# Optimization experiments

Measured on AMD Instinct MI355X. Metric: run time of the kernel, lower is better.

## Reference

```python
import jax, jax.numpy as jnp
import numpy as np
from jax import lax

B_, N_, DIM, HID, DST, NT, IR, DTR, HH, WW = 16, 4096, 192, 384, 16, 17, 128, 24, 64, 64


def _selective_scan(u, delta, A, Bs, Cs, D, delta_bias):
    # u, delta: (B, Din, L); A: (Din, N); Bs, Cs: (B, N, L); D, delta_bias: (Din,)
    delta = jax.nn.softplus(delta + delta_bias[None, :, None])
    dT = jnp.moveaxis(delta, 2, 0)   # (L, B, Din)
    uT = jnp.moveaxis(u, 2, 0)       # (L, B, Din)
    BT = jnp.moveaxis(Bs, 2, 0)      # (L, B, N)
    CT = jnp.moveaxis(Cs, 2, 0)      # (L, B, N)
    Bsz, Din, L = u.shape
    Nst = A.shape[1]
    h0 = jnp.zeros((Bsz, Din, Nst), u.dtype)

    def step(h, inp):
        d_l, u_l, b_l, c_l = inp
        da = jnp.exp(d_l[:, :, None] * A[None])              # (B, Din, N)
        h = da * h + (d_l * u_l)[:, :, None] * b_l[:, None, :]
        y = jnp.einsum('bdn,bn->bd', h, c_l)
        return h, y

    _, ys = lax.scan(step, h0, (dT, uT, BT, CT))
    y = jnp.moveaxis(ys, 0, 2)                               # (B, Din, L)
    return y + u * D[None, :, None]


def _assm_forward(x, token_weight, gumbel_noise, embB, route_w1, route_b1, route_w2,
                  route_b2, inproj_w, inproj_b, cpe_w, cpe_b, x_proj_w, dt_w, dt_b,
                  A_logs, Ds, norm_g, norm_b, outproj_w, outproj_b, H, W, gather_type):
    B, n, C = x.shape
    hidden = inproj_w.shape[0]
    dst = token_weight.shape[1]
    dtr = dt_w.shape[1]

    # routing + gumbel-softmax (hard, straight-through)
    full_emb = embB @ token_weight                           # (NT, d_state)
    hmid = jax.nn.gelu(x @ route_w1.T + route_b1)
    logits = jax.nn.log_softmax(hmid @ route_w2.T + route_b2, axis=-1)
    y_soft = jax.nn.softmax(logits + gumbel_noise, axis=-1)
    idx = jnp.argmax(y_soft, axis=-1)                        # (B, n)
    y_hard = jax.nn.one_hot(idx, logits.shape[-1], dtype=y_soft.dtype)
    cls_policy = y_hard + y_soft - lax.stop_gradient(y_soft)
    prompt = cls_policy @ full_emb                           # (B, n, d_state)

    det = lax.stop_gradient(idx)
    # (gather_type 3/5 keypoint-group remap omitted: gather_type == 1 here)
    sort_idx = jnp.argsort(det, axis=-1)                     # (B, n)
    inv_idx = jnp.argsort(sort_idx, axis=-1)                 # index_reverse

    # in_proj (1x1 conv == pointwise linear) then depthwise CPE gate
    xi = x @ inproj_w.T + inproj_b                           # (B, n, hidden)
    xg = xi.reshape(B, H, W, hidden).transpose(0, 3, 1, 2)   # NCHW
    cpe = lax.conv_general_dilated(xg, cpe_w, (1, 1), 'SAME',
                                   feature_group_count=hidden,
                                   dimension_numbers=('NCHW', 'OIHW', 'NCHW'))
    cpe = cpe + cpe_b[None, :, None, None]
    xg = xg * jax.nn.sigmoid(cpe)
    xflat = xg.reshape(B, hidden, n).transpose(0, 2, 1)      # (B, n, hidden)

    sem_x = jnp.take_along_axis(xflat, sort_idx[:, :, None], axis=1)

    # Selective_Scan core
    xs = sem_x.transpose(0, 2, 1)                            # (B, Din, L)
    x_dbl = jnp.einsum('bdl,cd->bcl', xs, x_proj_w)          # (B, dtr+2N, L)
    dts, Bs, Cs = jnp.split(x_dbl, [dtr, dtr + dst], axis=1)
    dts = jnp.einsum('brl,dr->bdl', dts, dt_w)
    if gather_type != 0:
        Cs = Cs + prompt.transpose(0, 2, 1)
    A = -jnp.exp(A_logs)
    y = _selective_scan(xs, dts, A, Bs, Cs, Ds, dt_b)        # (B, Din, L)
    y = y.transpose(0, 2, 1)                                 # (B, L, hidden)

    mu = jnp.mean(y, axis=-1, keepdims=True)
    var = jnp.mean(jnp.square(y - mu), axis=-1, keepdims=True)
    yn = (y - mu) / jnp.sqrt(var + 1e-5) * norm_g + norm_b
    out = yn @ outproj_w.T + outproj_b                       # (B, n, dim)
    out = jnp.take_along_axis(out, inv_idx[:, :, None], axis=1)
    return out


def setup_inputs() -> dict:
    key = jax.random.key(0)
    ks = jax.random.split(key, 16)

    def rn(k, sh, s=0.02):
        return jax.random.normal(k, sh, dtype=jnp.float32) * s

    u = jax.random.uniform(ks[0], (B_, N_, NT), jnp.float32, 1e-6, 1.0 - 1e-6)
    gumbel = -jnp.log(-jnp.log(u))

    # faithful dt bias init (inverse-softplus of log-uniform dt)
    rng = np.random.default_rng(0)
    dt = np.exp(rng.uniform(size=HID) * (np.log(0.1) - np.log(0.001)) + np.log(0.001))
    dt = np.clip(dt, 1e-4, None)
    inv_dt = dt + np.log(-np.expm1(-dt))

    A_logs = jnp.log(jnp.tile(jnp.arange(1, DST + 1, dtype=jnp.float32), (HID, 1)))

    return {
        'x': jax.random.normal(ks[1], (B_, N_, DIM), jnp.float32),
        'token_weight': rn(ks[2], (IR, DST), 0.1),
        'gumbel_noise': gumbel,
        'embB': jax.random.uniform(ks[3], (NT, IR), jnp.float32, -1.0 / NT, 1.0 / NT),
        'route_w1': rn(ks[4], (DIM // 3, DIM)),
        'route_b1': jnp.zeros((DIM // 3,), jnp.float32),
        'route_w2': rn(ks[5], (NT, DIM // 3)),
        'route_b2': jnp.zeros((NT,), jnp.float32),
        'inproj_w': rn(ks[6], (HID, DIM)),
        'inproj_b': jnp.zeros((HID,), jnp.float32),
        'cpe_w': rn(ks[7], (HID, 1, 3, 3), 0.1),
        'cpe_b': jnp.zeros((HID,), jnp.float32),
        'x_proj_w': rn(ks[8], (DTR + 2 * DST, HID)),
        'dt_w': jax.random.uniform(ks[9], (HID, DTR), jnp.float32, -DTR ** -0.5, DTR ** -0.5),
        'dt_b': jnp.asarray(inv_dt, jnp.float32),
        'A_logs': A_logs,
        'Ds': jnp.ones((HID,), jnp.float32),
        'norm_g': jnp.ones((HID,), jnp.float32),
        'norm_b': jnp.zeros((HID,), jnp.float32),
        'outproj_w': rn(ks[10], (DIM, HID)),
        'outproj_b': jnp.zeros((DIM,), jnp.float32),
        'H': HH,
        'W': WW,
        'gather_type': 1,
    }


def reference(x, token_weight, gumbel_noise, embB, route_w1, route_b1, route_w2,
              route_b2, inproj_w, inproj_b, cpe_w, cpe_b, x_proj_w, dt_w, dt_b,
              A_logs, Ds, norm_g, norm_b, outproj_w, outproj_b, H, W, gather_type):
    return _assm_forward(x, token_weight, gumbel_noise, embB, route_w1, route_b1,
                         route_w2, route_b2, inproj_w, inproj_b, cpe_w, cpe_b,
                         x_proj_w, dt_w, dt_b, A_logs, Ds, norm_g, norm_b,
                         outproj_w, outproj_b, H, W, gather_type)
```

## Files before the change

### kernel.cpp

```cpp
#include <hip/hip_runtime.h>
#include <math.h>

#define NB 16
#define NL 4096
#define ND 192
#define NH 384
#define NS 16
#define NTK 17
#define NIR 128
#define NR 24
#define NHH 64
#define NWW 64
#define NCHUNKS 64
#define CHUNKLEN 64
#define NTOK (NB*NL)

typedef __attribute__((ext_vector_type(8))) short short8;
typedef __attribute__((ext_vector_type(4))) float floatx4;

__device__ __forceinline__ float gelu_tanh(float x){
  return 0.5f*x*(1.0f + tanhf(0.7978845608028654f*(x + 0.044715f*x*x*x)));
}
__device__ __forceinline__ float softplus_f(float x){
  return (x > 20.0f) ? x : log1pf(expf(x));
}
__device__ __forceinline__ short f2bf(float f){
  unsigned u = __float_as_uint(f);
  unsigned r = (u + 0x7fffu + ((u >> 16) & 1u)) >> 16;
  return (short)r;
}

union Pack8 { uint4 v; short s[8]; };

__global__ void k_emb(const float* __restrict__ embB, const float* __restrict__ tw,
                      float* __restrict__ fe){
  for (int o = threadIdx.x; o < NTK*NS; o += 256){
    int t = o / NS, s = o % NS;
    float acc = 0.f;
    for (int i = 0; i < NIR; ++i) acc += embB[t*NIR+i]*tw[i*NS+s];
    fe[o] = acc;
  }
}

__global__ void k_cvtw(const float* __restrict__ inw, const float* __restrict__ ow,
                       const float* __restrict__ xpw, const float* __restrict__ dtw,
                       short* __restrict__ inwb, short* __restrict__ owb,
                       short* __restrict__ xpwb, short* __restrict__ dtwb){
  int i = blockIdx.x*256 + threadIdx.x;
  int stride = gridDim.x*256;
  for (int p = i; p < NH*ND; p += stride) inwb[p] = f2bf(inw[p]);
  for (int p = i; p < ND*NH; p += stride) owb[p] = f2bf(ow[p]);
  for (int p = i; p < 56*NH; p += stride) xpwb[p] = f2bf(xpw[p]);
  for (int p = i; p < NH*32; p += stride){
    int r = p >> 5, c = p & 31;
    dtwb[p] = (c < NR) ? f2bf(dtw[r*NR + c]) : (short)0;
  }
}

template<int EPI>
__global__ __launch_bounds__(256) void k_gemm(const float* __restrict__ A, int lda,
    const float* __restrict__ W, int ldw, const float* __restrict__ bias,
    float* __restrict__ C, int ldc, int N, int K){
  __shared__ float As[16][68];
  __shared__ float Ws[16][68];
  int tid = threadIdx.x;
  int m0 = blockIdx.x*64, n0 = blockIdx.y*64;
  int tx = tid & 15, ty = tid >> 4;
  int srow = tid >> 2, skseg = (tid & 3)*4;
  float acc[4][4] = {};
  for (int k0 = 0; k0 < K; k0 += 16){
    {
      const float* ap = A + (size_t)(m0+srow)*lda + k0 + skseg;
      float4 v = *(const float4*)ap;
      As[skseg+0][srow]=v.x; As[skseg+1][srow]=v.y;
      As[skseg+2][srow]=v.z; As[skseg+3][srow]=v.w;
    }
    {
      float4 v = {0.f,0.f,0.f,0.f};
      if (n0 + srow < N) v = *(const float4*)(W + (size_t)(n0+srow)*ldw + k0 + skseg);
      Ws[skseg+0][srow]=v.x; Ws[skseg+1][srow]=v.y;
      Ws[skseg+2][srow]=v.z; Ws[skseg+3][srow]=v.w;
    }
    __syncthreads();
    #pragma unroll
    for (int kk = 0; kk < 16; ++kk){
      float4 av = *(const float4*)&As[kk][ty*4];
      float4 wv = *(const float4*)&Ws[kk][tx*4];
      acc[0][0] += av.x*wv.x; acc[0][1] += av.x*wv.y;
      acc[0][2] += av.x*wv.z; acc[0][3] += av.x*wv.w;
      acc[1][0] += av.y*wv.x; acc[1][1] += av.y*wv.y;
      acc[1][2] += av.y*wv.z; acc[1][3] += av.y*wv.w;
      acc[2][0] += av.z*wv.x; acc[2][1] += av.z*wv.y;
      acc[2][2] += av.z*wv.z; acc[2][3] += av.z*wv.w;
      acc[3][0] += av.w*wv.x; acc[3][1] += av.w*wv.y;
      acc[3][2] += av.w*wv.z; acc[3][3] += av.w*wv.w;
    }
    __syncthreads();
  }
  #pragma unroll
  for (int i = 0; i < 4; ++i){
    int m = m0 + ty*4 + i;
    #pragma unroll
    for (int j = 0; j < 4; ++j){
      int n = n0 + tx*4 + j;
      if (n < N){
        float v = acc[i][j] + (bias ? bias[n] : 0.f);
        if (EPI==1) v = gelu_tanh(v);
        C[(size_t)m*ldc + n] = v;
      }
    }
  }
}

template<int EPI, int AF32, int LNA>
__global__ __launch_bounds__(256) void k_mfma(const void* __restrict__ Aptr, int lda,
    const short* __restrict__ Wbf, int ldw, const float* __restrict__ bias,
    float* __restrict__ C, int ldc, int N, int K, const int* __restrict__ remap,
    const float* __restrict__ lnm, const float* __restrict__ lnr,
    const float* __restrict__ lng, const float* __restrict__ lnb){
  __shared__ short As[128*40];
  __shared__ short Bs[64*40];
  int tid = threadIdx.x;
  int m0 = blockIdx.x*128, n0 = blockIdx.y*64;
  int w = tid >> 6, lane = tid & 63;
  int lq = lane >> 4, lr = lane & 15;
  floatx4 acc[2][4];
  #pragma unroll
  for (int i = 0; i < 2; ++i)
    #pragma unroll
    for (int j = 0; j < 4; ++j) acc[i][j] = (floatx4){0.f,0.f,0.f,0.f};
  int ar = tid >> 1, aq = (tid & 1)*2;
  int br = tid >> 2, bq = tid & 3;
  float mr = 0.f, rr = 0.f;
  if (LNA){ mr = lnm[m0+ar]; rr = lnr[m0+ar]; }
  for (int k0 = 0; k0 < K; k0 += 32){
    Pack8 sa0, sa1;
    if (AF32){
      const float* ap = (const float*)Aptr + (size_t)(m0+ar)*lda + k0 + aq*8;
      float f[16];
      float4 f0 = *(const float4*)(ap);
      float4 f1 = *(const float4*)(ap+4);
      float4 f2 = *(const float4*)(ap+8);
      float4 f3 = *(const float4*)(ap+12);
      f[0]=f0.x; f[1]=f0.y; f[2]=f0.z; f[3]=f0.w;
      f[4]=f1.x; f[5]=f1.y; f[6]=f1.z; f[7]=f1.w;
      f[8]=f2.x; f[9]=f2.y; f[10]=f2.z; f[11]=f2.w;
      f[12]=f3.x; f[13]=f3.y; f[14]=f3.z; f[15]=f3.w;
      if (LNA){
        const float* gp = lng + k0 + aq*8;
        const float* bp = lnb + k0 + aq*8;
        #pragma unroll
        for (int j = 0; j < 16; ++j) f[j] = (f[j]-mr)*rr*gp[j] + bp[j];
      }
      #pragma unroll
      for (int j = 0; j < 8; ++j){ sa0.s[j] = f2bf(f[j]); sa1.s[j] = f2bf(f[8+j]); }
    } else {
      const short* ap = (const short*)Aptr + (size_t)(m0+ar)*lda + k0 + aq*8;
      sa0.v = *(const uint4*)ap;
      sa1.v = *(const uint4*)(ap + 8);
    }
    uint4 bv = {0u,0u,0u,0u};
    if (n0 + br < N) bv = *(const uint4*)(Wbf + (size_t)(n0+br)*ldw + k0 + bq*8);
    __syncthreads();
    *(uint4*)&As[ar*40 + aq*8]     = sa0.v;
    *(uint4*)&As[ar*40 + aq*8 + 8] = sa1.v;
    *(uint4*)&Bs[br*40 + bq*8]     = bv;
    __syncthreads();
    short8 a0 = *(const short8*)&As[(w*32      + lr)*40 + lq*8];
    short8 a1 = *(const short8*)&As[(w*32 + 16 + lr)*40 + lq*8];
    short8 b0 = *(const short8*)&Bs[(     lr)*40 + lq*8];
    short8 b1 = *(const short8*)&Bs[(16 + lr)*40 + lq*8];
    short8 b2 = *(const short8*)&Bs[(32 + lr)*40 + lq*8];
    short8 b3 = *(const short8*)&Bs[(48 + lr)*40 + lq*8];
    acc[0][0] = __builtin_amdgcn_mfma_f32_16x16x32_bf16(a0, b0, acc[0][0], 0,0,0);
    acc[0][1] = __builtin_amdgcn_mfma_f32_16x16x32_bf16(a0, b1, acc[0][1], 0,0,0);
    acc[0][2] = __builtin_amdgcn_mfma_f32_16x16x32_bf16(a0, b2, acc[0][2], 0,0,0);
    acc[0][3] = __builtin_amdgcn_mfma_f32_16x16x32_bf16(a0, b3, acc[0][3], 0,0,0);
    acc[1][0] = __builtin_amdgcn_mfma_f32_16x16x32_bf16(a1, b0, acc[1][0], 0,0,0);
    acc[1][1] = __builtin_amdgcn_mfma_f32_16x16x32_bf16(a1, b1, acc[1][1], 0,0,0);
    acc[1][2] = __builtin_amdgcn_mfma_f32_16x16x32_bf16(a1, b2, acc[1][2], 0,0,0);
    acc[1][3] = __builtin_amdgcn_mfma_f32_16x16x32_bf16(a1, b3, acc[1][3], 0,0,0);
  }
  #pragma unroll
  for (int mt = 0; mt < 2; ++mt){
    #pragma unroll
    for (int r = 0; r < 4; ++r){
      int m = m0 + w*32 + mt*16 + lq*4 + r;
      int orow = (EPI==3) ? remap[m] : m;
      #pragma unroll
      for (int nt = 0; nt < 4; ++nt){
        int n = n0 + nt*16 + lr;
        if (n < N){
          float v = acc[mt][nt][r] + (bias ? bias[n] : 0.f);
          if (EPI==2) v = softplus_f(v);
          C[(size_t)orow*ldc + n] = v;
        }
      }
    }
  }
}

__global__ __launch_bounds__(256) void k_argmax(const float* __restrict__ hmid,
    const float* __restrict__ w2, const float* __restrict__ b2,
    const float* __restrict__ gumbel, int* __restrict__ idx){
  int g = blockIdx.x*256 + threadIdx.x;
  float hm[64];
  const float4* hp = (const float4*)(hmid + (size_t)g*64);
  #pragma unroll
  for (int i = 0; i < 16; ++i){
    float4 v = hp[i];
    hm[i*4+0]=v.x; hm[i*4+1]=v.y; hm[i*4+2]=v.z; hm[i*4+3]=v.w;
  }
  float best = -INFINITY; int bi = 0;
  for (int c = 0; c < NTK; ++c){
    float s = b2[c] + gumbel[(size_t)g*NTK + c];
    #pragma unroll
    for (int j = 0; j < 64; ++j) s += hm[j]*w2[c*64+j];
    if (s > best){ best = s; bi = c; }
  }
  idx[g] = bi;
}

__global__ __launch_bounds__(256) void k_sort(const int* __restrict__ idx,
    int* __restrict__ rmap, int* __restrict__ inv){
  int b = blockIdx.x, t = threadIdx.x;
  __shared__ int hist[NTK][256];
  __shared__ int tot[NTK];
  __shared__ int keybase[NTK];
  int keys[16];
  const int* ip = idx + b*NL + t*16;
  #pragma unroll
  for (int i = 0; i < 16; ++i) keys[i] = ip[i];
  #pragma unroll
  for (int k = 0; k < NTK; ++k){
    int c = 0;
    #pragma unroll
    for (int i = 0; i < 16; ++i) c += (keys[i]==k) ? 1 : 0;
    hist[k][t] = c;
  }
  __syncthreads();
  if (t < NTK){
    int run = 0;
    for (int j = 0; j < 256; ++j){ int v = hist[t][j]; hist[t][j] = run; run += v; }
    tot[t] = run;
  }
  __syncthreads();
  if (t == 0){
    int base = 0;
    for (int k = 0; k < NTK; ++k){ keybase[k] = base; base += tot[k]; }
  }
  __syncthreads();
  #pragma unroll
  for (int i = 0; i < 16; ++i){
    int k = keys[i];
    int cb = 0;
    #pragma unroll
    for (int j = 0; j < 16; ++j) cb += (j < i && keys[j]==k) ? 1 : 0;
    int pos = keybase[k] + hist[k][t] + cb;
    rmap[b*NL + pos] = b*NL + t*16 + i;
    inv[b*NL + t*16 + i] = pos;
  }
}

__global__ __launch_bounds__(384) void k_cpe(const float* __restrict__ xi,
    const float* __restrict__ cw, const float* __restrict__ cb,
    const int* __restrict__ inv, float* __restrict__ us){
  int bl = blockIdx.x;
  int cg = bl & 3;
  int xt = (bl>>2) & 7;
  int yt = (bl>>5) & 7;
  int b  = bl >> 8;
  __shared__ float tile[10*10*96];
  int tx = threadIdx.x;
  int ty = threadIdx.y;
  int c0 = cg*96;
  int ch = c0 + tx;
  for (int yy = 0; yy < 10; ++yy){
    int gy = yt*8 + yy - 1;
    for (int xx = ty; xx < 10; xx += 4){
      int gx = xt*8 + xx - 1;
      float v = 0.f;
      if (gy >= 0 && gy < NHH && gx >= 0 && gx < NWW)
        v = xi[((size_t)(b*NL + gy*NWW + gx))*NH + ch];
      tile[(yy*10 + xx)*96 + tx] = v;
    }
  }
  float wreg[9];
  #pragma unroll
  for (int j = 0; j < 9; ++j) wreg[j] = cw[ch*9 + j];
  float bias = cb[ch];
  __syncthreads();
  for (int yy = ty; yy < 8; yy += 4){
    #pragma unroll
    for (int xx = 0; xx < 8; ++xx){
      float acc = bias;
      #pragma unroll
      for (int dy = 0; dy < 3; ++dy)
        #pragma unroll
        for (int dx = 0; dx < 3; ++dx)
          acc += tile[((yy+dy)*10 + (xx+dx))*96 + tx] * wreg[dy*3+dx];
      float center = tile[((yy+1)*10 + (xx+1))*96 + tx];
      float gate = 1.f/(1.f + expf(-acc));
      int l = (yt*8+yy)*NWW + xt*8+xx;
      int pos = inv[b*NL + l];
      us[((size_t)(b*NL + pos))*NH + ch] = center*gate;
    }
  }
}

__global__ __launch_bounds__(256) void k_bc(const float* __restrict__ dbl,
    const int* __restrict__ idx, const float* __restrict__ fe,
    const int* __restrict__ gt, float* __restrict__ Bsb, float* __restrict__ Csb,
    short* __restrict__ dtsb){
  int g = blockIdx.x*256 + threadIdx.x;
  const float* dr = dbl + (size_t)g*56;
  int id = idx[g];
  int gather = gt[0];
  #pragma unroll
  for (int n = 0; n < NR; ++n) dtsb[(size_t)g*32 + n] = f2bf(dr[n]);
  #pragma unroll
  for (int n = NR; n < 32; ++n) dtsb[(size_t)g*32 + n] = 0;
  #pragma unroll
  for (int n = 0; n < NS; ++n){
    Bsb[(size_t)g*NS + n] = dr[24+n];
    float c = dr[40+n];
    if (gather != 0) c += fe[id*NS + n];
    Csb[(size_t)g*NS + n] = c;
  }
}

__device__ __forceinline__ void decay16(bool pw, float dlt, const float* An, float* a){
  if (pw){
    float r  = __expf(dlt*An[0]);
    float r2 = r*r;
    float r3 = r2*r;
    float r4 = r2*r2;
    float r8 = r4*r4;
    float r12 = r8*r4;
    a[0]=r;     a[1]=r2;     a[2]=r3;     a[3]=r4;
    a[4]=r4*r;  a[5]=r4*r2;  a[6]=r4*r3;  a[7]=r8;
    a[8]=r8*r;  a[9]=r8*r2;  a[10]=r8*r3; a[11]=r12;
    a[12]=r12*r; a[13]=r12*r2; a[14]=r12*r3; a[15]=r8*r8;
  } else {
    #pragma unroll
    for (int n = 0; n < NS; ++n) a[n] = __expf(dlt*An[n]);
  }
}
__device__ __forceinline__ bool pwcheck(const float* An){
  bool pw = true;
  #pragma unroll
  for (int n = 1; n < NS; ++n)
    pw = pw && (fabsf(An[n] - (n+1)*An[0]) <= 1e-4f*fabsf(An[n]));
  return pw;
}

__global__ __launch_bounds__(384) void k_scan1(const float* __restrict__ delta,
    const float* __restrict__ us, const float* __restrict__ Bsb,
    const float* __restrict__ A_logs, float* __restrict__ sds, float* __restrict__ Boff){
  int bc = blockIdx.x;
  int c = bc & (NCHUNKS-1);
  int b = bc >> 6;
  int d = threadIdx.x;
  __shared__ float4 Bsh[CHUNKLEN*4];
  int base = b*NL + c*CHUNKLEN;
  {
    const float4* Bg = (const float4*)(Bsb + (size_t)base*NS);
    for (int p = d; p < CHUNKLEN*4; p += 384) Bsh[p] = Bg[p];
  }
  float An[NS];
  #pragma unroll
  for (int n = 0; n < NS; ++n) An[n] = -expf(A_logs[d*NS + n]);
  bool pw = pwcheck(An);
  float h[NS];
  #pragma unroll
  for (int n = 0; n < NS; ++n) h[n]=0.f;
  float sd = 0.f;
  __syncthreads();
  size_t gi = (size_t)base*NH + d;
  float dlt = delta[gi];
  float uv  = us[gi];
  #pragma unroll 2
  for (int s = 0; s < CHUNKLEN; ++s){
    float dltc = dlt, uvc = uv;
    if (s < CHUNKLEN-1){
      dlt = delta[gi + NH];
      uv  = us[gi + NH];
    }
    float du = dltc*uvc;
    sd += dltc;
    float a[NS];
    decay16(pw, dltc, An, a);
    float bb[NS];
    #pragma unroll
    for (int q = 0; q < 4; ++q) *(float4*)&bb[4*q] = Bsh[s*4 + q];
    #pragma unroll
    for (int n = 0; n < NS; ++n) h[n] = a[n]*h[n] + du*bb[n];
    gi += NH;
  }
  sds[(size_t)bc*NH + d] = sd;
  size_t o = ((size_t)bc*NH + d)*NS;
  #pragma unroll
  for (int n = 0; n < NS; ++n) Boff[o+n] = h[n];
}

__global__ __launch_bounds__(256) void k_scan2(const float* __restrict__ A_logs,
    const float* __restrict__ sds, float* __restrict__ Boff){
  int i = blockIdx.x*256 + threadIdx.x;
  int dn = i % (NH*NS);
  int b = i / (NH*NS);
  float An = -expf(A_logs[dn]);
  float h = 0.f;
  for (int c = 0; c < NCHUNKS; ++c){
    int bc = b*NCHUNKS + c;
    float sd = sds[(size_t)bc*NH + (dn >> 4)];
    float a = __expf(sd*An);
    size_t o = (size_t)bc*(NH*NS) + dn;
    float bo = Boff[o];
    Boff[o] = h;
    h = a*h + bo;
  }
}

__global__ __launch_bounds__(384) void k_scan3(const float* __restrict__ delta,
    const float* __restrict__ Bsb, const float* __restrict__ Csb,
    const float* __restrict__ A_logs, const float* __restrict__ Ds,
    const float* __restrict__ hinit, float* __restrict__ us){
  int bc = blockIdx.x;
  int c = bc & (NCHUNKS-1);
  int b = bc >> 6;
  int d = threadIdx.x;
  __shared__ float4 Bsh[CHUNKLEN*4];
  __shared__ float4 Csh[CHUNKLEN*4];
  int base = b*NL + c*CHUNKLEN;
  {
    const float4* Bg = (const float4*)(Bsb + (size_t)base*NS);
    const float4* Cg = (const float4*)(Csb + (size_t)base*NS);
    for (int p = d; p < CHUNKLEN*4; p += 384){
      Bsh[p] = Bg[p];
      Csh[p] = Cg[p];
    }
  }
  float An[NS];
  #pragma unroll
  for (int n = 0; n < NS; ++n) An[n] = -expf(A_logs[d*NS + n]);
  bool pw = pwcheck(An);
  float h[NS];
  size_t ho = ((size_t)bc*NH + d)*NS;
  #pragma unroll
  for (int n = 0; n < NS; ++n) h[n] = hinit[ho + n];
  float Dd = Ds[d];
  __syncthreads();
  size_t gi = (size_t)base*NH + d;
  float dlt = delta[gi];
  float uv  = us[gi];
  #pragma unroll 2
  for (int s = 0; s < CHUNKLEN; ++s){
    float dltc = dlt, uvc = uv;
    if (s < CHUNKLEN-1){
      dlt = delta[gi + NH];
      uv  = us[gi + NH];
    }
    float du = dltc*uvc;
    float a[NS];
    decay16(pw, dltc, An, a);
    float bb[NS], cc[NS];
    #pragma unroll
    for (int q = 0; q < 4; ++q){
      *(float4*)&bb[4*q] = Bsh[s*4 + q];
      *(float4*)&cc[4*q] = Csh[s*4 + q];
    }
    #pragma unroll
    for (int n = 0; n < NS; ++n) h[n] = a[n]*h[n] + du*bb[n];
    float ya = 0.f, yb = 0.f, yc = 0.f, yd = 0.f;
    #pragma unroll
    for (int q = 0; q < 4; ++q){
      ya += h[q]*cc[q];
      yb += h[4+q]*cc[4+q];
      yc += h[8+q]*cc[8+q];
      yd += h[12+q]*cc[12+q];
    }
    float y = (ya+yb)+(yc+yd);
    us[gi] = y + uvc*Dd;
    gi += NH;
  }
}

__global__ __launch_bounds__(256) void k_lnstat(const float* __restrict__ y,
    float* __restrict__ mean, float* __restrict__ rstd){
  int g = blockIdx.x*4 + (threadIdx.x >> 6);
  int lane = threadIdx.x & 63;
  size_t ro = (size_t)g*NH;
  float v[6];
  #pragma unroll
  for (int i = 0; i < 6; ++i) v[i] = y[ro + i*64 + lane];
  float s = 0.f;
  #pragma unroll
  for (int i = 0; i < 6; ++i) s += v[i];
  #pragma unroll
  for (int off = 32; off > 0; off >>= 1) s += __shfl_xor(s, off);
  float mu = s * (1.f/NH);
  float vs = 0.f;
  #pragma unroll
  for (int i = 0; i < 6; ++i){ float d = v[i]-mu; vs += d*d; }
  #pragma unroll
  for (int off = 32; off > 0; off >>= 1) vs += __shfl_xor(vs, off);
  float rs = rsqrtf(vs*(1.f/NH) + 1e-5f);
  if (lane == 0){ mean[g] = mu; rstd[g] = rs; }
}

extern "C" void kernel_launch(void* const* d_in, const int* in_sizes, int n_in,
                              void* d_out, int out_size, void* d_ws, size_t ws_size,
                              hipStream_t stream){
  const float* x      = (const float*)d_in[0];
  const float* tw     = (const float*)d_in[1];
  const float* gumbel = (const float*)d_in[2];
  const float* embB   = (const float*)d_in[3];
  const float* rw1    = (const float*)d_in[4];
  const float* rb1    = (const float*)d_in[5];
  const float* rw2    = (const float*)d_in[6];
  const float* rb2    = (const float*)d_in[7];
  const float* inw    = (const float*)d_in[8];
  const float* inb    = (const float*)d_in[9];
  const float* cw     = (const float*)d_in[10];
  const float* cb     = (const float*)d_in[11];
  const float* xpw    = (const float*)d_in[12];
  const float* dtw    = (const float*)d_in[13];
  const float* dtb    = (const float*)d_in[14];
  const float* A_logs = (const float*)d_in[15];
  const float* Ds     = (const float*)d_in[16];
  const float* ng     = (const float*)d_in[17];
  const float* nbv    = (const float*)d_in[18];
  const float* ow     = (const float*)d_in[19];
  const float* ob     = (const float*)d_in[20];
  const int*   gt     = (const int*)d_in[23];
  float* out = (float*)d_out;

  float* ws = (float*)d_ws;
  size_t o = 0;
  float* fe   = ws + o; o += 512;
  int* idx    = (int*)(ws + o); o += NTOK;
  int* rmap   = (int*)(ws + o); o += NTOK;
  int* inv    = (int*)(ws + o); o += NTOK;
  float* hmid = ws + o; o += (size_t)NTOK*64;
  float* xi   = ws + o; o += (size_t)NTOK*NH;
  float* us   = ws + o; o += (size_t)NTOK*NH;
  float* Bsb  = ws + o; o += (size_t)NTOK*NS;
  float* Csb  = ws + o; o += (size_t)NTOK*NS;
  float* sds  = ws + o; o += (size_t)NB*NCHUNKS*NH;
  float* Bof  = ws + o; o += (size_t)NB*NCHUNKS*NH*NS;
  short* inwb = (short*)(ws + o); o += (NH*ND)/2;
  short* owb  = (short*)(ws + o); o += (ND*NH)/2;
  short* xpwb = (short*)(ws + o); o += (56*NH)/2 + 32;
  short* dtwb = (short*)(ws + o); o += (NH*32)/2;
  float* dbl = hmid;
  float* delta = xi;
  short* dtsb = (short*)Bof;
  float* lnmean = (float*)idx;
  float* lnrstd = (float*)inv;

  k_emb<<<1,256,0,stream>>>(embB, tw, fe);
  k_cvtw<<<64,256,0,stream>>>(inw, ow, xpw, dtw, inwb, owb, xpwb, dtwb);
  k_gemm<1><<<dim3(NTOK/64,1),256,0,stream>>>(x, ND, rw1, ND, rb1, hmid, 64, 64, ND);
  k_argmax<<<NTOK/256,256,0,stream>>>(hmid, rw2, rb2, gumbel, idx);
  k_sort<<<NB,256,0,stream>>>(idx, rmap, inv);
  k_mfma<0,1,0><<<dim3(NTOK/128,6),256,0,stream>>>(x, ND, inwb, ND, inb, xi, NH, NH, ND,
      nullptr, nullptr, nullptr, nullptr, nullptr);
  k_cpe<<<NB*64*4,dim3(96,4),0,stream>>>(xi, cw, cb, inv, us);
  k_mfma<0,1,0><<<dim3(NTOK/128,1),256,0,stream>>>(us, NH, xpwb, NH, nullptr, dbl, 56, 56, NH,
      nullptr, nullptr, nullptr, nullptr, nullptr);
  k_bc<<<NTOK/256,256,0,stream>>>(dbl, idx, fe, gt, Bsb, Csb, dtsb);
  k_mfma<2,0,0><<<dim3(NTOK/128,6),256,0,stream>>>(dtsb, 32, dtwb, 32, dtb, delta, NH, NH, 32,
      nullptr, nullptr, nullptr, nullptr, nullptr);
  k_scan1<<<NB*NCHUNKS,384,0,stream>>>(delta, us, Bsb, A_logs, sds, Bof);
  k_scan2<<<(NB*NH*NS)/256,256,0,stream>>>(A_logs, sds, Bof);
  k_scan3<<<NB*NCHUNKS,384,0,stream>>>(delta, Bsb, Csb, A_logs, Ds, Bof, us);
  k_lnstat<<<NTOK/4,256,0,stream>>>(us, lnmean, lnrstd);
  k_mfma<3,1,1><<<dim3(NTOK/128,3),256,0,stream>>>(us, NH, owb, NH, ob, out, ND, ND, NH,
      rmap, lnmean, lnrstd, ng, nbv);
}
```

Before: 747.3 us.

## Use longer scan chunks, vectorize chunk-state I/O, fold emb kernel into weight convert

Halves the number of scan chunks (chunk length 64 to 128), which halves the chunk-carry traffic through Boff/sds and the serial length of the middle pass, but also halves the block count of the two chunk-scan kernels (512 blocks of 384 threads). Stores and loads the 16-element per-thread state with float4 instead of scalars. Also merges the tiny embedding matmul into the weight-conversion kernel to remove one launch.

```diff
diff --git a/kernel.cpp b/kernel.cpp
--- a/kernel.cpp
+++ b/kernel.cpp
@@ -11,8 +11,8 @@
 #define NR 24
 #define NHH 64
 #define NWW 64
-#define NCHUNKS 64
-#define CHUNKLEN 64
+#define NCHUNKS 32
+#define CHUNKLEN 128
 #define NTOK (NB*NL)
 
 typedef __attribute__((ext_vector_type(8))) short short8;
@@ -32,20 +32,12 @@
 
 union Pack8 { uint4 v; short s[8]; };
 
-__global__ void k_emb(const float* __restrict__ embB, const float* __restrict__ tw,
-                      float* __restrict__ fe){
-  for (int o = threadIdx.x; o < NTK*NS; o += 256){
-    int t = o / NS, s = o % NS;
-    float acc = 0.f;
-    for (int i = 0; i < NIR; ++i) acc += embB[t*NIR+i]*tw[i*NS+s];
-    fe[o] = acc;
-  }
-}
-
 __global__ void k_cvtw(const float* __restrict__ inw, const float* __restrict__ ow,
                        const float* __restrict__ xpw, const float* __restrict__ dtw,
                        short* __restrict__ inwb, short* __restrict__ owb,
-                       short* __restrict__ xpwb, short* __restrict__ dtwb){
+                       short* __restrict__ xpwb, short* __restrict__ dtwb,
+                       const float* __restrict__ embB, const float* __restrict__ tw,
+                       float* __restrict__ fe){
   int i = blockIdx.x*256 + threadIdx.x;
   int stride = gridDim.x*256;
   for (int p = i; p < NH*ND; p += stride) inwb[p] = f2bf(inw[p]);
@@ -54,6 +46,14 @@
   for (int p = i; p < NH*32; p += stride){
     int r = p >> 5, c = p & 31;
     dtwb[p] = (c < NR) ? f2bf(dtw[r*NR + c]) : (short)0;
+  }
+  if (blockIdx.x == 0){
+    for (int o = threadIdx.x; o < NTK*NS; o += 256){
+      int t = o / NS, s = o % NS;
+      float acc = 0.f;
+      for (int k = 0; k < NIR; ++k) acc += embB[t*NIR+k]*tw[k*NS+s];
+      fe[o] = acc;
+    }
   }
 }
 
@@ -359,7 +359,7 @@
     const float* __restrict__ A_logs, float* __restrict__ sds, float* __restrict__ Boff){
   int bc = blockIdx.x;
   int c = bc & (NCHUNKS-1);
-  int b = bc >> 6;
+  int b = bc >> 5;
   int d = threadIdx.x;
   __shared__ float4 Bsh[CHUNKLEN*4];
   int base = b*NL + c*CHUNKLEN;
@@ -399,8 +399,10 @@
   }
   sds[(size_t)bc*NH + d] = sd;
   size_t o = ((size_t)bc*NH + d)*NS;
-  #pragma unroll
-  for (int n = 0; n < NS; ++n) Boff[o+n] = h[n];
+  *(float4*)(Boff + o)      = make_float4(h[0], h[1], h[2], h[3]);
+  *(float4*)(Boff + o + 4)  = make_float4(h[4], h[5], h[6], h[7]);
+  *(float4*)(Boff + o + 8)  = make_float4(h[8], h[9], h[10],h[11]);
+  *(float4*)(Boff + o + 12) = make_float4(h[12],h[13],h[14],h[15]);
 }
 
 __global__ __launch_bounds__(256) void k_scan2(const float* __restrict__ A_logs,
@@ -409,10 +411,11 @@
   int dn = i % (NH*NS);
   int b = i / (NH*NS);
   float An = -expf(A_logs[dn]);
+  int d = dn >> 4;
   float h = 0.f;
   for (int c = 0; c < NCHUNKS; ++c){
     int bc = b*NCHUNKS + c;
-    float sd = sds[(size_t)bc*NH + (dn >> 4)];
+    float sd = sds[(size_t)bc*NH + d];
     float a = __expf(sd*An);
     size_t o = (size_t)bc*(NH*NS) + dn;
     float bo = Boff[o];
@@ -427,7 +430,7 @@
     const float* __restrict__ hinit, float* __restrict__ us){
   int bc = blockIdx.x;
   int c = bc & (NCHUNKS-1);
-  int b = bc >> 6;
+  int b = bc >> 5;
   int d = threadIdx.x;
   __shared__ float4 Bsh[CHUNKLEN*4];
   __shared__ float4 Csh[CHUNKLEN*4];
@@ -446,8 +449,16 @@
   bool pw = pwcheck(An);
   float h[NS];
   size_t ho = ((size_t)bc*NH + d)*NS;
-  #pragma unroll
-  for (int n = 0; n < NS; ++n) h[n] = hinit[ho + n];
+  {
+    float4 h0 = *(const float4*)(hinit + ho);
+    float4 h1 = *(const float4*)(hinit + ho + 4);
+    float4 h2 = *(const float4*)(hinit + ho + 8);
+    float4 h3 = *(const float4*)(hinit + ho + 12);
+    h[0]=h0.x; h[1]=h0.y; h[2]=h0.z; h[3]=h0.w;
+    h[4]=h1.x; h[5]=h1.y; h[6]=h1.z; h[7]=h1.w;
+    h[8]=h2.x; h[9]=h2.y; h[10]=h2.z; h[11]=h2.w;
+    h[12]=h3.x; h[13]=h3.y; h[14]=h3.z; h[15]=h3.w;
+  }
   float Dd = Ds[d];
   __syncthreads();
   size_t gi = (size_t)base*NH + d;
@@ -558,8 +569,7 @@
   float* lnmean = (float*)idx;
   float* lnrstd = (float*)inv;
 
-  k_emb<<<1,256,0,stream>>>(embB, tw, fe);
-  k_cvtw<<<64,256,0,stream>>>(inw, ow, xpw, dtw, inwb, owb, xpwb, dtwb);
+  k_cvtw<<<64,256,0,stream>>>(inw, ow, xpw, dtw, inwb, owb, xpwb, dtwb, embB, tw, fe);
   k_gemm<1><<<dim3(NTOK/64,1),256,0,stream>>>(x, ND, rw1, ND, rb1, hmid, 64, 64, ND);
   k_argmax<<<NTOK/256,256,0,stream>>>(hmid, rw2, rb2, gumbel, idx);
   k_sort<<<NB,256,0,stream>>>(idx, rmap, inv);
```

Result: faster. 726.8 us (-2.7%).
